# Kernel tuning notes

Measured on AMD Instinct MI355X. Metric: run time of the kernel, lower is better.

Reference implementation:

```python
import jax, jax.numpy as jnp
import numpy as np

B, C, CI, H, W = 4, 64, 32, 96, 96  # batch, in_channels, inter_channels, height, width


def conv2d(x, w, b, stride=1, pad=0):
    out = jax.lax.conv_general_dilated(
        x, w, (stride, stride), [(pad, pad), (pad, pad)],
        dimension_numbers=('NCHW', 'OIHW', 'NCHW'))
    return out + b[None, :, None, None]


def maxpool2(x):
    return jax.lax.reduce_window(x, -jnp.inf, jax.lax.max, (1, 1, 2, 2), (1, 1, 2, 2), 'VALID')


def up2(x):
    return jnp.repeat(jnp.repeat(x, 2, axis=2), 2, axis=3)


def bn_train(x, gamma, beta, eps=1e-5):
    # BatchNorm2d in training mode: batch statistics over (N, H, W)
    m = jnp.mean(x, axis=(0, 2, 3), keepdims=True)
    v = jnp.var(x, axis=(0, 2, 3), keepdims=True)
    return gamma[None, :, None, None] * (x - m) * jax.lax.rsqrt(v + eps) + beta[None, :, None, None]


def setup_inputs() -> dict:
    key = jax.random.key(0)
    ks = jax.random.split(key, 20)
    s1 = (2.0 / C) ** 0.5            # kaiming-ish for 1x1 convs
    s3 = (2.0 / (C * 9)) ** 0.5      # kaiming-ish for 3x3 convs
    sw = (2.0 / CI) ** 0.5
    return {
        'x':         jax.random.normal(ks[0], (B, C, H, W), jnp.float32),
        'x_pan':     jax.random.normal(ks[1], (B, C, H, W), jnp.float32),
        'g_w':       jax.random.normal(ks[2], (CI, C, 1, 1), jnp.float32) * s1,
        'g_b':       jnp.zeros((CI,), jnp.float32),
        'g_pan_w':   jax.random.normal(ks[3], (CI, C, 1, 1), jnp.float32) * s1,
        'g_pan_b':   jnp.zeros((CI,), jnp.float32),
        'theta_w':   jax.random.normal(ks[4], (CI, C, 3, 3), jnp.float32) * s3,
        'theta_b':   jax.random.normal(ks[5], (CI,), jnp.float32) * 0.02,
        'phi_w':     jax.random.normal(ks[6], (CI, C, 3, 3), jnp.float32) * s3,
        'phi_b':     jax.random.normal(ks[7], (CI,), jnp.float32) * 0.02,
        'phi_pan_w': jax.random.normal(ks[8], (CI, C, 3, 3), jnp.float32) * s3,
        'phi_pan_b': jax.random.normal(ks[9], (CI,), jnp.float32) * 0.02,
        'W_w':       jax.random.normal(ks[10], (C, CI, 1, 1), jnp.float32) * sw,
        'W_b':       jnp.zeros((C,), jnp.float32),
        'W_gamma':   jnp.ones((C,), jnp.float32),
        'W_beta':    jnp.zeros((C,), jnp.float32),
        'Wp_w':      jax.random.normal(ks[11], (C, CI, 1, 1), jnp.float32) * sw,
        'Wp_b':      jnp.zeros((C,), jnp.float32),
        'Wp_gamma':  jnp.ones((C,), jnp.float32),
        'Wp_beta':   jnp.zeros((C,), jnp.float32),
    }


def reference(x, x_pan, g_w, g_b, g_pan_w, g_pan_b, theta_w, theta_b,
              phi_w, phi_b, phi_pan_w, phi_pan_b,
              W_w, W_b, W_gamma, W_beta, Wp_w, Wp_b, Wp_gamma, Wp_beta):
    b = x.shape[0]
    # self branch
    g_x = maxpool2(conv2d(x, g_w, g_b)).reshape(b, CI, -1)                           # (B,CI,M)
    theta = up2(conv2d(x, theta_w, theta_b, stride=2, pad=1)).reshape(b, CI, -1)     # (B,CI,N)
    phi = up2(maxpool2(conv2d(x, phi_w, phi_b, stride=2, pad=1))).reshape(b, CI, -1) # (B,CI,M)
    f = jnp.einsum('bcn,bcm->bnm', theta, phi)                                       # (B,N,M)
    a = jax.nn.softmax(f, axis=-1)
    y = jnp.einsum('bnm,bcm->bcn', a, g_x).reshape(b, CI, H, W)
    W_y = bn_train(conv2d(y, W_w, W_b), W_gamma, W_beta)
    # cross-modal (pan) branch, sharing theta queries
    g_p = maxpool2(conv2d(x_pan, g_pan_w, g_pan_b)).reshape(b, CI, -1)
    phi_p = up2(maxpool2(conv2d(x_pan, phi_pan_w, phi_pan_b, stride=2, pad=1))).reshape(b, CI, -1)
    f_p = jnp.einsum('bcn,bcm->bnm', theta, phi_p)
    a_p = jax.nn.softmax(f_p, axis=-1)
    y_p = jnp.einsum('bnm,bcm->bcn', a_p, g_p).reshape(b, CI, H, W)
    Wp_y = bn_train(conv2d(y_p, Wp_w, Wp_b), Wp_gamma, Wp_beta)
    return jnp.concatenate([W_y, Wp_y], axis=1)  # (B, 2C, H, W)
```

## Files before the change

### kernel.cpp

```cpp
#include <hip/hip_runtime.h>
#include <math.h>

#define BB   4
#define CIN  64
#define CMID 32
#define HS   96
#define WS   96
#define H2   48
#define W2   48
#define H4   24
#define W4   24
#define N2   (H2*W2)
#define M4   (H4*W4)

__global__ __launch_bounds__(256) void conv3x3_kernel(
    const float* __restrict__ x, const float* __restrict__ x_pan,
    const float* __restrict__ theta_w, const float* __restrict__ theta_b,
    const float* __restrict__ phi_w,   const float* __restrict__ phi_b,
    const float* __restrict__ phi_pan_w, const float* __restrict__ phi_pan_b,
    float* __restrict__ T, float* __restrict__ Kp)
{
    const int p  = blockIdx.x;
    const int b  = blockIdx.y;
    const int cz = blockIdx.z;

    const float* xin  = (cz == 2) ? x_pan : x;
    const float* wgt  = (cz == 0) ? theta_w : (cz == 1 ? phi_w : phi_pan_w);
    const float* bias = (cz == 0) ? theta_b : (cz == 1 ? phi_b : phi_pan_b);

    __shared__ __align__(16) float xs[16][5][112];
    __shared__ float wsm[16][9][32];

    const int tid = threadIdx.x;
    const int co  = tid & 31;
    const int g   = tid >> 5;

    float acc[2][6];
    #pragma unroll
    for (int o = 0; o < 2; ++o)
        #pragma unroll
        for (int j = 0; j < 6; ++j) acc[o][j] = 0.f;

    const int row0 = 4*p - 1;

    for (int ci0 = 0; ci0 < CIN; ci0 += 16) {
        __syncthreads();
        for (int idx = tid; idx < 16*5*112; idx += 256) {
            int ci  = idx / (5*112);
            int rem = idx % (5*112);
            int rr  = rem / 112, cc = rem % 112;
            int row = row0 + rr, col = cc - 8;
            float v = 0.f;
            if (row >= 0 && row < HS && col >= 0 && col < WS)
                v = xin[((b*CIN + ci0 + ci)*HS + row)*WS + col];
            xs[ci][rr][cc] = v;
        }
        for (int idx = tid; idx < 16*9*32; idx += 256) {
            int c2 = idx & 31;
            int kk = (idx >> 5) % 9;
            int ci = idx / (9*32);
            wsm[ci][kk][c2] = wgt[(c2*CIN + ci0 + ci)*9 + kk];
        }
        __syncthreads();

        for (int ci = 0; ci < 16; ++ci) {
            float w9[9];
            #pragma unroll
            for (int kk = 0; kk < 9; ++kk) w9[kk] = wsm[ci][kk][co];

            #pragma unroll
            for (int rr = 0; rr < 5; ++rr) {
                const float4* xr = (const float4*)&xs[ci][rr][12*g + 4];
                float4 t0 = xr[0], t1 = xr[1], t2 = xr[2], t3 = xr[3];
                float xv[16] = {t0.x,t0.y,t0.z,t0.w, t1.x,t1.y,t1.z,t1.w,
                                t2.x,t2.y,t2.z,t2.w, t3.x,t3.y,t3.z,t3.w};
                if (rr <= 2) {
                    const int kh = rr;
                    #pragma unroll
                    for (int j = 0; j < 6; ++j)
                        #pragma unroll
                        for (int kw = 0; kw < 3; ++kw)
                            acc[0][j] += w9[kh*3+kw] * xv[3 + 2*j + kw];
                }
                if (rr >= 2) {
                    const int kh = rr - 2;
                    #pragma unroll
                    for (int j = 0; j < 6; ++j)
                        #pragma unroll
                        for (int kw = 0; kw < 3; ++kw)
                            acc[1][j] += w9[kh*3+kw] * xv[3 + 2*j + kw];
                }
            }
        }
    }

    const float bv = bias[co];
    if (cz == 0) {
        #pragma unroll
        for (int o = 0; o < 2; ++o)
            #pragma unroll
            for (int j = 0; j < 6; ++j)
                T[((b*CMID + co)*H2 + (2*p + o))*W2 + (6*g + j)] = acc[o][j] + bv;
    } else {
        #pragma unroll
        for (int j3 = 0; j3 < 3; ++j3) {
            float m = fmaxf(fmaxf(acc[0][2*j3], acc[0][2*j3+1]),
                            fmaxf(acc[1][2*j3], acc[1][2*j3+1]));
            Kp[((((cz-1)*BB + b)*CMID + co)*H4 + p)*W4 + (3*g + j3)] = m + bv;
        }
    }
}

__global__ __launch_bounds__(256) void gconv_kernel(
    const float* __restrict__ x, const float* __restrict__ x_pan,
    const float* __restrict__ g_w, const float* __restrict__ g_b,
    const float* __restrict__ g_pan_w, const float* __restrict__ g_pan_b,
    float* __restrict__ Vv)
{
    const int r4 = blockIdx.x;
    const int bb = blockIdx.y;
    const int br = bb >> 2, b = bb & 3;
    const float* xin = br ? x_pan : x;
    const float* wg  = br ? g_pan_w : g_w;
    const float* bg  = br ? g_pan_b : g_b;

    __shared__ float wl[CIN][CMID];
    const int tid = threadIdx.x;
    for (int idx = tid; idx < CIN*CMID; idx += 256) {
        int c = idx >> 6, ci = idx & 63;
        wl[ci][c] = wg[idx];
    }
    __syncthreads();

    const int c  = tid & 31;
    const int sg = tid >> 5;

    float acc[3][4][4];
    #pragma unroll
    for (int s = 0; s < 3; ++s)
        #pragma unroll
        for (int r = 0; r < 4; ++r)
            #pragma unroll
            for (int d = 0; d < 4; ++d) acc[s][r][d] = 0.f;

    for (int ci = 0; ci < CIN; ++ci) {
        const float wv = wl[ci][c];
        const float* xbase = &xin[((b*CIN + ci)*HS + 4*r4)*WS + 12*sg];
        #pragma unroll
        for (int r = 0; r < 4; ++r) {
            const float4* xp = (const float4*)(xbase + r*WS);
            #pragma unroll
            for (int s = 0; s < 3; ++s) {
                float4 xv = xp[s];
                acc[s][r][0] += wv*xv.x; acc[s][r][1] += wv*xv.y;
                acc[s][r][2] += wv*xv.z; acc[s][r][3] += wv*xv.w;
            }
        }
    }

    const float bv = bg[c];
    #pragma unroll
    for (int s = 0; s < 3; ++s) {
        float m00 = fmaxf(fmaxf(acc[s][0][0], acc[s][0][1]), fmaxf(acc[s][1][0], acc[s][1][1]));
        float m01 = fmaxf(fmaxf(acc[s][0][2], acc[s][0][3]), fmaxf(acc[s][1][2], acc[s][1][3]));
        float m10 = fmaxf(fmaxf(acc[s][2][0], acc[s][2][1]), fmaxf(acc[s][3][0], acc[s][3][1]));
        float m11 = fmaxf(fmaxf(acc[s][2][2], acc[s][2][3]), fmaxf(acc[s][3][2], acc[s][3][3]));
        Vv[((bb*CMID + c)*H4 + r4)*W4 + (3*sg + s)] = 0.25f*(m00+m01+m10+m11) + bv;
    }
}

__global__ __launch_bounds__(256) void attn_kernel(
    const float* __restrict__ T, const float* __restrict__ Kp,
    const float* __restrict__ Vv, float* __restrict__ Y)
{
    const int qt = blockIdx.x;
    const int bb = blockIdx.y;
    const int b  = bb & 3;

    __shared__ float smem[256*37];
    __shared__ float pmax[16][16];

    const int tid = threadIdx.x;
    const int ql  = tid & 15;
    const int ks  = tid >> 4;
    const int q   = qt*16 + ql;

    float qv[32];
    const float* Tb = T + b*CMID*N2;
    #pragma unroll
    for (int c = 0; c < 32; ++c) qv[c] = Tb[c*N2 + q];

    const float* Kb = Kp + bb*CMID*M4;
    const float* Vb = Vv + bb*CMID*M4;
    float* myss = &smem[tid*37];

    float m = -1e30f;
    for (int j = 0; j < 36; j += 4) {
        const int k = ks*36 + j;
        float s0 = 0.f, s1 = 0.f, s2 = 0.f, s3 = 0.f;
        #pragma unroll
        for (int c = 0; c < 32; ++c) {
            float4 kv = *(const float4*)&Kb[c*M4 + k];
            s0 += qv[c]*kv.x; s1 += qv[c]*kv.y; s2 += qv[c]*kv.z; s3 += qv[c]*kv.w;
        }
        myss[j] = s0; myss[j+1] = s1; myss[j+2] = s2; myss[j+3] = s3;
        m = fmaxf(m, fmaxf(fmaxf(s0, s1), fmaxf(s2, s3)));
    }
    pmax[ks][ql] = m;
    __syncthreads();
    float M = pmax[0][ql];
    #pragma unroll
    for (int i = 1; i < 16; ++i) M = fmaxf(M, pmax[i][ql]);

    float zp = 0.f;
    float av[32];
    #pragma unroll
    for (int c = 0; c < 32; ++c) av[c] = 0.f;
    for (int j = 0; j < 36; j += 4) {
        const int k = ks*36 + j;
        float p0 = __expf(myss[j]   - M);
        float p1 = __expf(myss[j+1] - M);
        float p2 = __expf(myss[j+2] - M);
        float p3 = __expf(myss[j+3] - M);
        zp += (p0 + p1) + (p2 + p3);
        #pragma unroll
        for (int c = 0; c < 32; ++c) {
            float4 vv = *(const float4*)&Vb[c*M4 + k];
            av[c] += p0*vv.x + p1*vv.y + p2*vv.z + p3*vv.w;
        }
    }
    __syncthreads();

    #pragma unroll
    for (int c = 0; c < 32; ++c) smem[tid*33 + c] = av[c];
    smem[256*33 + tid] = zp;
    __syncthreads();

    float Z = 0.f;
    #pragma unroll
    for (int i = 0; i < 16; ++i) Z += smem[256*33 + i*16 + ql];
    const float inv = 1.0f / Z;
    float* Yb = Y + bb*CMID*N2;
    #pragma unroll
    for (int cc = 0; cc < 2; ++cc) {
        const int c = ks*2 + cc;
        float sum = 0.f;
        #pragma unroll
        for (int i = 0; i < 16; ++i) sum += smem[(i*16 + ql)*33 + c];
        Yb[c*N2 + q] = sum * inv;
    }
}

__global__ __launch_bounds__(256) void wbn_kernel(
    const float* __restrict__ Y,
    const float* __restrict__ W_w, const float* __restrict__ W_b,
    const float* __restrict__ W_gamma, const float* __restrict__ W_beta,
    const float* __restrict__ Wp_w, const float* __restrict__ Wp_b,
    const float* __restrict__ Wp_gamma, const float* __restrict__ Wp_beta,
    float* __restrict__ out)
{
    const int og = blockIdx.x;
    const int br = og >> 6, o = og & 63;
    const float* Ww = br ? Wp_w : W_w;
    const float  bias = (br ? Wp_b : W_b)[o];
    const float* Ybase = Y + br*BB*CMID*N2;

    float wreg[32];
    #pragma unroll
    for (int c = 0; c < 32; ++c) wreg[c] = Ww[o*CMID + c];

    __shared__ float rbuf[256];
    const int tid = threadIdx.x;

    float4 zloc[9];
    float psum = 0.f;
    #pragma unroll
    for (int i = 0; i < 9; ++i) {
        const int g4 = tid + 256*i;
        const int b  = g4 / 576;
        const int n4 = (g4 % 576) * 4;
        const float* yb = Ybase + b*CMID*N2 + n4;
        float4 a = {0.f, 0.f, 0.f, 0.f};
        #pragma unroll
        for (int c = 0; c < 32; ++c) {
            float4 yv = *(const float4*)&yb[c*N2];
            a.x += wreg[c]*yv.x; a.y += wreg[c]*yv.y;
            a.z += wreg[c]*yv.z; a.w += wreg[c]*yv.w;
        }
        a.x += bias; a.y += bias; a.z += bias; a.w += bias;
        zloc[i] = a;
        psum += (a.x + a.y) + (a.z + a.w);
    }

    rbuf[tid] = psum;
    __syncthreads();
    for (int sft = 128; sft > 0; sft >>= 1) {
        if (tid < sft) rbuf[tid] += rbuf[tid + sft];
        __syncthreads();
    }
    const float mean = rbuf[0] * (1.0f/9216.0f);
    __syncthreads();

    float pvar = 0.f;
    #pragma unroll
    for (int i = 0; i < 9; ++i) {
        float4 a = zloc[i];
        float d0 = a.x - mean, d1 = a.y - mean, d2 = a.z - mean, d3 = a.w - mean;
        pvar += (d0*d0 + d1*d1) + (d2*d2 + d3*d3);
    }
    rbuf[tid] = pvar;
    __syncthreads();
    for (int sft = 128; sft > 0; sft >>= 1) {
        if (tid < sft) rbuf[tid] += rbuf[tid + sft];
        __syncthreads();
    }
    const float var = rbuf[0] * (1.0f/9216.0f);

    const float gamma = (br ? Wp_gamma : W_gamma)[o];
    const float beta  = (br ? Wp_beta  : W_beta)[o];
    const float scale = gamma * rsqrtf(var + 1e-5f);
    const float shift = beta - mean*scale;

    #pragma unroll
    for (int i = 0; i < 9; ++i) {
        const int g4 = tid + 256*i;
        const int b  = g4 / 576;
        const int nn = (g4 % 576) * 4;
        const int r  = nn / W2, s = nn % W2;
        float4 a = zloc[i];
        float v0 = a.x*scale + shift, v1 = a.y*scale + shift;
        float v2 = a.z*scale + shift, v3 = a.w*scale + shift;
        float4 lo = {v0, v0, v1, v1};
        float4 hi = {v2, v2, v3, v3};
        float* ob = out + ((size_t)(b*128 + og)*HS + 2*r)*WS + 2*s;
        *(float4*)(ob)        = lo;
        *(float4*)(ob + 4)    = hi;
        *(float4*)(ob + WS)   = lo;
        *(float4*)(ob + WS+4) = hi;
    }
}

extern "C" void kernel_launch(void* const* d_in, const int* in_sizes, int n_in,
                              void* d_out, int out_size, void* d_ws, size_t ws_size,
                              hipStream_t stream) {
    (void)in_sizes; (void)n_in; (void)out_size; (void)ws_size;
    const float* x         = (const float*)d_in[0];
    const float* x_pan     = (const float*)d_in[1];
    const float* g_w       = (const float*)d_in[2];
    const float* g_b       = (const float*)d_in[3];
    const float* g_pan_w   = (const float*)d_in[4];
    const float* g_pan_b   = (const float*)d_in[5];
    const float* theta_w   = (const float*)d_in[6];
    const float* theta_b   = (const float*)d_in[7];
    const float* phi_w     = (const float*)d_in[8];
    const float* phi_b     = (const float*)d_in[9];
    const float* phi_pan_w = (const float*)d_in[10];
    const float* phi_pan_b = (const float*)d_in[11];
    const float* W_w       = (const float*)d_in[12];
    const float* W_b       = (const float*)d_in[13];
    const float* W_gamma   = (const float*)d_in[14];
    const float* W_beta    = (const float*)d_in[15];
    const float* Wp_w      = (const float*)d_in[16];
    const float* Wp_b      = (const float*)d_in[17];
    const float* Wp_gamma  = (const float*)d_in[18];
    const float* Wp_beta   = (const float*)d_in[19];

    float* out = (float*)d_out;
    float* ws  = (float*)d_ws;

    float* T  = ws;
    float* Kp = T  + BB*CMID*N2;
    float* Vv = Kp + 2*BB*CMID*M4;
    float* Yw = Vv + 2*BB*CMID*M4;

    conv3x3_kernel<<<dim3(24, BB, 3), 256, 0, stream>>>(
        x, x_pan, theta_w, theta_b, phi_w, phi_b, phi_pan_w, phi_pan_b, T, Kp);
    gconv_kernel<<<dim3(24, 8), 256, 0, stream>>>(
        x, x_pan, g_w, g_b, g_pan_w, g_pan_b, Vv);
    attn_kernel<<<dim3(144, 8), 256, 0, stream>>>(T, Kp, Vv, Yw);
    wbn_kernel<<<dim3(128), 256, 0, stream>>>(
        Yw, W_w, W_b, W_gamma, W_beta, Wp_w, Wp_b, Wp_gamma, Wp_beta, out);
}
```

Measured before the change: 400.6 us.

## Restructure conv, attention and BN kernels for more parallelism and register reuse

The theta conv now computes only the needed stride-2 rows and writes T in a query-major layout. The phi convs are split by input-channel halves into partial buffers, which a new phipool kernel sums, max-pools and biases. The g conv stages inputs in shared memory over a larger grid. The attention kernel keeps scores in registers and reduces with wave shuffles instead of large shared arrays. The W conv plus BN is split into a parallel conv-with-partial-stats kernel and a normalize-and-upsample kernel using a sum/sum-of-squares variance. Together these are meant to raise occupancy and spread work over more blocks, at the cost of extra launches, intermediate traffic, and a less numerically stable variance formula.

```diff
diff --git a/kernel.cpp b/kernel.cpp
--- a/kernel.cpp
+++ b/kernel.cpp
@@ -16,17 +16,12 @@
 __global__ __launch_bounds__(256) void conv3x3_kernel(
     const float* __restrict__ x, const float* __restrict__ x_pan,
     const float* __restrict__ theta_w, const float* __restrict__ theta_b,
-    const float* __restrict__ phi_w,   const float* __restrict__ phi_b,
-    const float* __restrict__ phi_pan_w, const float* __restrict__ phi_pan_b,
-    float* __restrict__ T, float* __restrict__ Kp)
-{
-    const int p  = blockIdx.x;
+    const float* __restrict__ phi_w, const float* __restrict__ phi_pan_w,
+    float* __restrict__ T, float* __restrict__ Pphi)
+{
+    const int bx = blockIdx.x;
     const int b  = blockIdx.y;
     const int cz = blockIdx.z;
-
-    const float* xin  = (cz == 2) ? x_pan : x;
-    const float* wgt  = (cz == 0) ? theta_w : (cz == 1 ? phi_w : phi_pan_w);
-    const float* bias = (cz == 0) ? theta_b : (cz == 1 ? phi_b : phi_pan_b);
 
     __shared__ __align__(16) float xs[16][5][112];
     __shared__ float wsm[16][9][32];
@@ -35,141 +30,205 @@
     const int co  = tid & 31;
     const int g   = tid >> 5;
 
-    float acc[2][6];
-    #pragma unroll
-    for (int o = 0; o < 2; ++o)
-        #pragma unroll
-        for (int j = 0; j < 6; ++j) acc[o][j] = 0.f;
-
-    const int row0 = 4*p - 1;
-
-    for (int ci0 = 0; ci0 < CIN; ci0 += 16) {
-        __syncthreads();
-        for (int idx = tid; idx < 16*5*112; idx += 256) {
-            int ci  = idx / (5*112);
-            int rem = idx % (5*112);
-            int rr  = rem / 112, cc = rem % 112;
-            int row = row0 + rr, col = cc - 8;
-            float v = 0.f;
-            if (row >= 0 && row < HS && col >= 0 && col < WS)
-                v = xin[((b*CIN + ci0 + ci)*HS + row)*WS + col];
-            xs[ci][rr][cc] = v;
-        }
-        for (int idx = tid; idx < 16*9*32; idx += 256) {
-            int c2 = idx & 31;
-            int kk = (idx >> 5) % 9;
-            int ci = idx / (9*32);
-            wsm[ci][kk][c2] = wgt[(c2*CIN + ci0 + ci)*9 + kk];
-        }
-        __syncthreads();
-
-        for (int ci = 0; ci < 16; ++ci) {
-            float w9[9];
-            #pragma unroll
-            for (int kk = 0; kk < 9; ++kk) w9[kk] = wsm[ci][kk][co];
-
-            #pragma unroll
-            for (int rr = 0; rr < 5; ++rr) {
-                const float4* xr = (const float4*)&xs[ci][rr][12*g + 4];
-                float4 t0 = xr[0], t1 = xr[1], t2 = xr[2], t3 = xr[3];
-                float xv[16] = {t0.x,t0.y,t0.z,t0.w, t1.x,t1.y,t1.z,t1.w,
-                                t2.x,t2.y,t2.z,t2.w, t3.x,t3.y,t3.z,t3.w};
-                if (rr <= 2) {
-                    const int kh = rr;
+    const float* xin = (cz == 2) ? x_pan : x;
+    const float* wgt = (cz == 0) ? theta_w : (cz == 1 ? phi_w : phi_pan_w);
+
+    if (cz == 0) {
+        const int p = bx;
+        const int row0 = 2*p - 1;
+        float acc[6] = {0.f,0.f,0.f,0.f,0.f,0.f};
+
+        for (int ci0 = 0; ci0 < 64; ci0 += 16) {
+            __syncthreads();
+            for (int u = tid; u < 16*3*28; u += 256) {
+                int ci = u / 84, rem = u % 84, rr = rem / 28, k = rem % 28;
+                int row = row0 + rr;
+                float4 v = {0.f,0.f,0.f,0.f};
+                if (row >= 0 && k >= 2 && k <= 25)
+                    v = *(const float4*)&xin[((b*64 + ci0 + ci)*96 + row)*96 + 4*k - 8];
+                *(float4*)&xs[ci][rr][4*k] = v;
+            }
+            for (int u = tid; u < 1152; u += 256) {
+                int c2 = u / 36, f = u % 36;
+                float4 wv = *(const float4*)&wgt[c2*576 + ci0*9 + 4*f];
+                int lin = 4*f;
+                wsm[(lin  )/9][(lin  )%9][c2] = wv.x;
+                wsm[(lin+1)/9][(lin+1)%9][c2] = wv.y;
+                wsm[(lin+2)/9][(lin+2)%9][c2] = wv.z;
+                wsm[(lin+3)/9][(lin+3)%9][c2] = wv.w;
+            }
+            __syncthreads();
+
+            for (int ci = 0; ci < 16; ++ci) {
+                float w9[9];
+                #pragma unroll
+                for (int kk = 0; kk < 9; ++kk) w9[kk] = wsm[ci][kk][co];
+                #pragma unroll
+                for (int rr = 0; rr < 3; ++rr) {
+                    const float4* xr = (const float4*)&xs[ci][rr][12*g + 4];
+                    float4 t0 = xr[0], t1 = xr[1], t2 = xr[2], t3 = xr[3];
+                    float xv[16] = {t0.x,t0.y,t0.z,t0.w, t1.x,t1.y,t1.z,t1.w,
+                                    t2.x,t2.y,t2.z,t2.w, t3.x,t3.y,t3.z,t3.w};
                     #pragma unroll
                     for (int j = 0; j < 6; ++j)
                         #pragma unroll
                         for (int kw = 0; kw < 3; ++kw)
-                            acc[0][j] += w9[kh*3+kw] * xv[3 + 2*j + kw];
+                            acc[j] += w9[rr*3+kw] * xv[3 + 2*j + kw];
                 }
-                if (rr >= 2) {
-                    const int kh = rr - 2;
-                    #pragma unroll
-                    for (int j = 0; j < 6; ++j)
+            }
+        }
+        const float bv = theta_b[co];
+        #pragma unroll
+        for (int j = 0; j < 6; ++j)
+            T[(b*N2 + p*48 + 6*g + j)*32 + co] = acc[j] + bv;
+    } else {
+        const int p = bx >> 1, half = bx & 1;
+        const int row0 = 4*p - 1;
+        float acc[2][6];
+        #pragma unroll
+        for (int o = 0; o < 2; ++o)
+            #pragma unroll
+            for (int j = 0; j < 6; ++j) acc[o][j] = 0.f;
+
+        for (int cih = 0; cih < 2; ++cih) {
+            const int ci0 = half*32 + cih*16;
+            __syncthreads();
+            for (int u = tid; u < 16*5*28; u += 256) {
+                int ci = u / 140, rem = u % 140, rr = rem / 28, k = rem % 28;
+                int row = row0 + rr;
+                float4 v = {0.f,0.f,0.f,0.f};
+                if (row >= 0 && k >= 2 && k <= 25)
+                    v = *(const float4*)&xin[((b*64 + ci0 + ci)*96 + row)*96 + 4*k - 8];
+                *(float4*)&xs[ci][rr][4*k] = v;
+            }
+            for (int u = tid; u < 1152; u += 256) {
+                int c2 = u / 36, f = u % 36;
+                float4 wv = *(const float4*)&wgt[c2*576 + ci0*9 + 4*f];
+                int lin = 4*f;
+                wsm[(lin  )/9][(lin  )%9][c2] = wv.x;
+                wsm[(lin+1)/9][(lin+1)%9][c2] = wv.y;
+                wsm[(lin+2)/9][(lin+2)%9][c2] = wv.z;
+                wsm[(lin+3)/9][(lin+3)%9][c2] = wv.w;
+            }
+            __syncthreads();
+
+            for (int ci = 0; ci < 16; ++ci) {
+                float w9[9];
+                #pragma unroll
+                for (int kk = 0; kk < 9; ++kk) w9[kk] = wsm[ci][kk][co];
+                #pragma unroll
+                for (int rr = 0; rr < 5; ++rr) {
+                    const float4* xr = (const float4*)&xs[ci][rr][12*g + 4];
+                    float4 t0 = xr[0], t1 = xr[1], t2 = xr[2], t3 = xr[3];
+                    float xv[16] = {t0.x,t0.y,t0.z,t0.w, t1.x,t1.y,t1.z,t1.w,
+                                    t2.x,t2.y,t2.z,t2.w, t3.x,t3.y,t3.z,t3.w};
+                    if (rr <= 2) {
                         #pragma unroll
-                        for (int kw = 0; kw < 3; ++kw)
-                            acc[1][j] += w9[kh*3+kw] * xv[3 + 2*j + kw];
+                        for (int j = 0; j < 6; ++j)
+                            #pragma unroll
+                            for (int kw = 0; kw < 3; ++kw)
+                                acc[0][j] += w9[rr*3+kw] * xv[3 + 2*j + kw];
+                    }
+                    if (rr >= 2) {
+                        #pragma unroll
+                        for (int j = 0; j < 6; ++j)
+                            #pragma unroll
+                            for (int kw = 0; kw < 3; ++kw)
+                                acc[1][j] += w9[(rr-2)*3+kw] * xv[3 + 2*j + kw];
+                    }
                 }
             }
         }
-    }
-
-    const float bv = bias[co];
-    if (cz == 0) {
+        const int brn = cz - 1;
+        float* Pb = Pphi + (size_t)(((half*2 + brn)*4 + b)*32 + co)*N2;
         #pragma unroll
         for (int o = 0; o < 2; ++o)
             #pragma unroll
             for (int j = 0; j < 6; ++j)
-                T[((b*CMID + co)*H2 + (2*p + o))*W2 + (6*g + j)] = acc[o][j] + bv;
-    } else {
-        #pragma unroll
-        for (int j3 = 0; j3 < 3; ++j3) {
-            float m = fmaxf(fmaxf(acc[0][2*j3], acc[0][2*j3+1]),
-                            fmaxf(acc[1][2*j3], acc[1][2*j3+1]));
-            Kp[((((cz-1)*BB + b)*CMID + co)*H4 + p)*W4 + (3*g + j3)] = m + bv;
-        }
-    }
-}
-
-__global__ __launch_bounds__(256) void gconv_kernel(
+                Pb[(2*p + o)*48 + 6*g + j] = acc[o][j];
+    }
+}
+
+__global__ __launch_bounds__(256) void phipool_kernel(
+    const float* __restrict__ Pphi,
+    const float* __restrict__ phi_b, const float* __restrict__ phi_pan_b,
+    float* __restrict__ Kp)
+{
+    const int o = blockIdx.x*256 + threadIdx.x;
+    const int br   = o / 73728;
+    const int rem  = o % 73728;
+    const int b    = rem / 18432;
+    const int rem2 = rem % 18432;
+    const int co   = rem2 / 576;
+    const int rem3 = rem2 % 576;
+    const int pr   = rem3 / 24, pc = rem3 % 24;
+
+    const int h1 = 2*4*32*N2;
+    const int base = (((br*4 + b)*32 + co)*48 + 2*pr)*48 + 2*pc;
+    float2 a0 = *(const float2*)&Pphi[base];
+    float2 a1 = *(const float2*)&Pphi[base + 48];
+    float2 c0 = *(const float2*)&Pphi[h1 + base];
+    float2 c1 = *(const float2*)&Pphi[h1 + base + 48];
+    float v00 = a0.x + c0.x, v01 = a0.y + c0.y;
+    float v10 = a1.x + c1.x, v11 = a1.y + c1.y;
+    float bv = (br ? phi_pan_b : phi_b)[co];
+    Kp[o] = fmaxf(fmaxf(v00, v01), fmaxf(v10, v11)) + bv;
+}
+
+__global__ __launch_bounds__(384) void gconv_kernel(
     const float* __restrict__ x, const float* __restrict__ x_pan,
     const float* __restrict__ g_w, const float* __restrict__ g_b,
     const float* __restrict__ g_pan_w, const float* __restrict__ g_pan_b,
     float* __restrict__ Vv)
 {
     const int r4 = blockIdx.x;
-    const int bb = blockIdx.y;
+    const int ch = blockIdx.y;
+    const int bb = blockIdx.z;
     const int br = bb >> 2, b = bb & 3;
     const float* xin = br ? x_pan : x;
     const float* wg  = br ? g_pan_w : g_w;
-    const float* bg  = br ? g_pan_b : g_b;
-
-    __shared__ float wl[CIN][CMID];
+
+    __shared__ __align__(16) float xs[32][4][48];
+    __shared__ float wl[64*33];
     const int tid = threadIdx.x;
-    for (int idx = tid; idx < CIN*CMID; idx += 256) {
-        int c = idx >> 6, ci = idx & 63;
-        wl[ci][c] = wg[idx];
-    }
-    __syncthreads();
+    for (int u = tid; u < 2048; u += 384) {
+        int c2 = u >> 6, ci = u & 63;
+        wl[ci*33 + c2] = wg[u];
+    }
 
     const int c  = tid & 31;
-    const int sg = tid >> 5;
-
-    float acc[3][4][4];
-    #pragma unroll
-    for (int s = 0; s < 3; ++s)
-        #pragma unroll
-        for (int r = 0; r < 4; ++r)
-            #pragma unroll
-            for (int d = 0; d < 4; ++d) acc[s][r][d] = 0.f;
-
-    for (int ci = 0; ci < CIN; ++ci) {
-        const float wv = wl[ci][c];
-        const float* xbase = &xin[((b*CIN + ci)*HS + 4*r4)*WS + 12*sg];
-        #pragma unroll
-        for (int r = 0; r < 4; ++r) {
-            const float4* xp = (const float4*)(xbase + r*WS);
-            #pragma unroll
-            for (int s = 0; s < 3; ++s) {
-                float4 xv = xp[s];
-                acc[s][r][0] += wv*xv.x; acc[s][r][1] += wv*xv.y;
-                acc[s][r][2] += wv*xv.z; acc[s][r][3] += wv*xv.w;
-            }
-        }
-    }
-
-    const float bv = bg[c];
-    #pragma unroll
-    for (int s = 0; s < 3; ++s) {
-        float m00 = fmaxf(fmaxf(acc[s][0][0], acc[s][0][1]), fmaxf(acc[s][1][0], acc[s][1][1]));
-        float m01 = fmaxf(fmaxf(acc[s][0][2], acc[s][0][3]), fmaxf(acc[s][1][2], acc[s][1][3]));
-        float m10 = fmaxf(fmaxf(acc[s][2][0], acc[s][2][1]), fmaxf(acc[s][3][0], acc[s][3][1]));
-        float m11 = fmaxf(fmaxf(acc[s][2][2], acc[s][2][3]), fmaxf(acc[s][3][2], acc[s][3][3]));
-        Vv[((bb*CMID + c)*H4 + r4)*W4 + (3*sg + s)] = 0.25f*(m00+m01+m10+m11) + bv;
-    }
-}
-
-__global__ __launch_bounds__(256) void attn_kernel(
+    const int sl = tid >> 5;
+    float4 ac0 = {0,0,0,0}, ac1 = {0,0,0,0}, ac2 = {0,0,0,0}, ac3 = {0,0,0,0};
+
+    for (int ci0 = 0; ci0 < 64; ci0 += 32) {
+        __syncthreads();
+        for (int u = tid; u < 32*4*12; u += 384) {
+            int ci = u / 48, rem = u % 48, r = rem / 12, k = rem % 12;
+            *(float4*)&xs[ci][r][4*k] =
+                *(const float4*)&xin[((b*64 + ci0 + ci)*96 + 4*r4 + r)*96 + ch*48 + 4*k];
+        }
+        __syncthreads();
+        for (int ci = 0; ci < 32; ++ci) {
+            const float wv = wl[(ci0 + ci)*33 + c];
+            float4 x0 = *(const float4*)&xs[ci][0][4*sl];
+            float4 x1 = *(const float4*)&xs[ci][1][4*sl];
+            float4 x2 = *(const float4*)&xs[ci][2][4*sl];
+            float4 x3 = *(const float4*)&xs[ci][3][4*sl];
+            ac0.x += wv*x0.x; ac0.y += wv*x0.y; ac0.z += wv*x0.z; ac0.w += wv*x0.w;
+            ac1.x += wv*x1.x; ac1.y += wv*x1.y; ac1.z += wv*x1.z; ac1.w += wv*x1.w;
+            ac2.x += wv*x2.x; ac2.y += wv*x2.y; ac2.z += wv*x2.z; ac2.w += wv*x2.w;
+            ac3.x += wv*x3.x; ac3.y += wv*x3.y; ac3.z += wv*x3.z; ac3.w += wv*x3.w;
+        }
+    }
+    float m00 = fmaxf(fmaxf(ac0.x, ac0.y), fmaxf(ac1.x, ac1.y));
+    float m01 = fmaxf(fmaxf(ac0.z, ac0.w), fmaxf(ac1.z, ac1.w));
+    float m10 = fmaxf(fmaxf(ac2.x, ac2.y), fmaxf(ac3.x, ac3.y));
+    float m11 = fmaxf(fmaxf(ac2.z, ac2.w), fmaxf(ac3.z, ac3.w));
+    float bv = (br ? g_pan_b : g_b)[c];
+    Vv[(bb*32 + c)*576 + r4*24 + ch*12 + sl] = 0.25f*(m00+m01+m10+m11) + bv;
+}
+
+__global__ __launch_bounds__(256, 4) void attn_kernel(
     const float* __restrict__ T, const float* __restrict__ Kp,
     const float* __restrict__ Vv, float* __restrict__ Y)
 {
@@ -177,167 +236,170 @@
     const int bb = blockIdx.y;
     const int b  = bb & 3;
 
-    __shared__ float smem[256*37];
-    __shared__ float pmax[16][16];
-
-    const int tid = threadIdx.x;
-    const int ql  = tid & 15;
-    const int ks  = tid >> 4;
-    const int q   = qt*16 + ql;
+    __shared__ float mbuf[64];
+    __shared__ float zbuf[64];
+    __shared__ float avbuf[4*16*33];
+
+    const int tid  = threadIdx.x;
+    const int ql   = tid & 15;
+    const int ks   = tid >> 4;
+    const int q    = qt*16 + ql;
+    const int lane = tid & 63;
+    const int w    = tid >> 6;
 
     float qv[32];
-    const float* Tb = T + b*CMID*N2;
-    #pragma unroll
-    for (int c = 0; c < 32; ++c) qv[c] = Tb[c*N2 + q];
-
-    const float* Kb = Kp + bb*CMID*M4;
-    const float* Vb = Vv + bb*CMID*M4;
-    float* myss = &smem[tid*37];
-
+    const float4* Tq = (const float4*)(T + (size_t)(b*N2 + q)*32);
+    #pragma unroll
+    for (int i = 0; i < 8; ++i) {
+        float4 t = Tq[i];
+        qv[4*i] = t.x; qv[4*i+1] = t.y; qv[4*i+2] = t.z; qv[4*i+3] = t.w;
+    }
+
+    const float* Kb = Kp + (size_t)bb*32*576;
+    const float* Vb = Vv + (size_t)bb*32*576;
+
+    float sc[36];
     float m = -1e30f;
-    for (int j = 0; j < 36; j += 4) {
-        const int k = ks*36 + j;
+    #pragma unroll
+    for (int jj = 0; jj < 9; ++jj) {
+        const int k0 = ks*36 + 4*jj;
         float s0 = 0.f, s1 = 0.f, s2 = 0.f, s3 = 0.f;
         #pragma unroll
-        for (int c = 0; c < 32; ++c) {
-            float4 kv = *(const float4*)&Kb[c*M4 + k];
-            s0 += qv[c]*kv.x; s1 += qv[c]*kv.y; s2 += qv[c]*kv.z; s3 += qv[c]*kv.w;
-        }
-        myss[j] = s0; myss[j+1] = s1; myss[j+2] = s2; myss[j+3] = s3;
+        for (int c2 = 0; c2 < 32; ++c2) {
+            float4 kv = *(const float4*)&Kb[c2*576 + k0];
+            s0 += qv[c2]*kv.x; s1 += qv[c2]*kv.y; s2 += qv[c2]*kv.z; s3 += qv[c2]*kv.w;
+        }
+        sc[4*jj] = s0; sc[4*jj+1] = s1; sc[4*jj+2] = s2; sc[4*jj+3] = s3;
         m = fmaxf(m, fmaxf(fmaxf(s0, s1), fmaxf(s2, s3)));
     }
-    pmax[ks][ql] = m;
+    m = fmaxf(m, __shfl_xor(m, 16));
+    m = fmaxf(m, __shfl_xor(m, 32));
+    if (lane < 16) mbuf[w*16 + ql] = m;
     __syncthreads();
-    float M = pmax[0][ql];
-    #pragma unroll
-    for (int i = 1; i < 16; ++i) M = fmaxf(M, pmax[i][ql]);
-
+    const float M = fmaxf(fmaxf(mbuf[ql], mbuf[16+ql]),
+                          fmaxf(mbuf[32+ql], mbuf[48+ql]));
+
+    float av[32];
+    #pragma unroll
+    for (int c2 = 0; c2 < 32; ++c2) av[c2] = 0.f;
     float zp = 0.f;
-    float av[32];
-    #pragma unroll
-    for (int c = 0; c < 32; ++c) av[c] = 0.f;
-    for (int j = 0; j < 36; j += 4) {
-        const int k = ks*36 + j;
-        float p0 = __expf(myss[j]   - M);
-        float p1 = __expf(myss[j+1] - M);
-        float p2 = __expf(myss[j+2] - M);
-        float p3 = __expf(myss[j+3] - M);
+    #pragma unroll
+    for (int jj = 0; jj < 9; ++jj) {
+        const int k0 = ks*36 + 4*jj;
+        float p0 = __expf(sc[4*jj]   - M);
+        float p1 = __expf(sc[4*jj+1] - M);
+        float p2 = __expf(sc[4*jj+2] - M);
+        float p3 = __expf(sc[4*jj+3] - M);
         zp += (p0 + p1) + (p2 + p3);
         #pragma unroll
-        for (int c = 0; c < 32; ++c) {
-            float4 vv = *(const float4*)&Vb[c*M4 + k];
-            av[c] += p0*vv.x + p1*vv.y + p2*vv.z + p3*vv.w;
-        }
+        for (int c2 = 0; c2 < 32; ++c2) {
+            float4 vv = *(const float4*)&Vb[c2*576 + k0];
+            av[c2] += p0*vv.x + p1*vv.y + p2*vv.z + p3*vv.w;
+        }
+    }
+    zp += __shfl_xor(zp, 16); zp += __shfl_xor(zp, 32);
+    #pragma unroll
+    for (int c2 = 0; c2 < 32; ++c2) {
+        av[c2] += __shfl_xor(av[c2], 16);
+        av[c2] += __shfl_xor(av[c2], 32);
+    }
+    if (lane < 16) {
+        #pragma unroll
+        for (int c2 = 0; c2 < 32; ++c2) avbuf[(w*16 + ql)*33 + c2] = av[c2];
+        zbuf[w*16 + ql] = zp;
     }
     __syncthreads();
 
-    #pragma unroll
-    for (int c = 0; c < 32; ++c) smem[tid*33 + c] = av[c];
-    smem[256*33 + tid] = zp;
-    __syncthreads();
-
-    float Z = 0.f;
-    #pragma unroll
-    for (int i = 0; i < 16; ++i) Z += smem[256*33 + i*16 + ql];
+    const float Z = zbuf[ql] + zbuf[16+ql] + zbuf[32+ql] + zbuf[48+ql];
     const float inv = 1.0f / Z;
-    float* Yb = Y + bb*CMID*N2;
+    float* Yb = Y + (size_t)bb*32*N2;
     #pragma unroll
     for (int cc = 0; cc < 2; ++cc) {
-        const int c = ks*2 + cc;
-        float sum = 0.f;
-        #pragma unroll
-        for (int i = 0; i < 16; ++i) sum += smem[(i*16 + ql)*33 + c];
-        Yb[c*N2 + q] = sum * inv;
-    }
-}
-
-__global__ __launch_bounds__(256) void wbn_kernel(
+        const int c2 = 2*ks + cc;
+        float s = avbuf[ql*33 + c2] + avbuf[(16+ql)*33 + c2]
+                + avbuf[(32+ql)*33 + c2] + avbuf[(48+ql)*33 + c2];
+        Yb[c2*N2 + q] = s * inv;
+    }
+}
+
+__global__ __launch_bounds__(192) void wconv_kernel(
     const float* __restrict__ Y,
     const float* __restrict__ W_w, const float* __restrict__ W_b,
+    const float* __restrict__ Wp_w, const float* __restrict__ Wp_b,
+    float* __restrict__ zbuf, float* __restrict__ Psum, float* __restrict__ Psq)
+{
+    const int og = blockIdx.x, b = blockIdx.y;
+    const int br = og >> 6, o = og & 63;
+    const float* Ww = br ? Wp_w : W_w;
+    const float bias = (br ? Wp_b : W_b)[o];
+    const float* yb = Y + (size_t)(br*4 + b)*32*N2;
+
+    float wreg[32];
+    #pragma unroll
+    for (int c2 = 0; c2 < 32; ++c2) wreg[c2] = Ww[o*32 + c2];
+
+    const int tid = threadIdx.x;
+    float ps = 0.f, pq = 0.f;
+    float* zb = zbuf + (size_t)(og*4 + b)*N2;
+    #pragma unroll
+    for (int i = 0; i < 3; ++i) {
+        const int g = tid + 192*i;
+        float4 a = {bias, bias, bias, bias};
+        #pragma unroll
+        for (int c2 = 0; c2 < 32; ++c2) {
+            float4 yv = *(const float4*)&yb[c2*N2 + 4*g];
+            a.x += wreg[c2]*yv.x; a.y += wreg[c2]*yv.y;
+            a.z += wreg[c2]*yv.z; a.w += wreg[c2]*yv.w;
+        }
+        *(float4*)&zb[4*g] = a;
+        ps += (a.x + a.y) + (a.z + a.w);
+        pq += (a.x*a.x + a.y*a.y) + (a.z*a.z + a.w*a.w);
+    }
+    #pragma unroll
+    for (int d = 1; d < 64; d <<= 1) {
+        ps += __shfl_xor(ps, d);
+        pq += __shfl_xor(pq, d);
+    }
+    __shared__ float sb[3], qb[3];
+    const int lane = tid & 63, w = tid >> 6;
+    if (lane == 0) { sb[w] = ps; qb[w] = pq; }
+    __syncthreads();
+    if (tid == 0) {
+        Psum[og*4 + b] = sb[0] + sb[1] + sb[2];
+        Psq[og*4 + b]  = qb[0] + qb[1] + qb[2];
+    }
+}
+
+__global__ __launch_bounds__(576) void bnup_kernel(
+    const float* __restrict__ zbuf,
+    const float* __restrict__ Psum, const float* __restrict__ Psq,
     const float* __restrict__ W_gamma, const float* __restrict__ W_beta,
-    const float* __restrict__ Wp_w, const float* __restrict__ Wp_b,
     const float* __restrict__ Wp_gamma, const float* __restrict__ Wp_beta,
     float* __restrict__ out)
 {
-    const int og = blockIdx.x;
+    const int og = blockIdx.x, b = blockIdx.y;
     const int br = og >> 6, o = og & 63;
-    const float* Ww = br ? Wp_w : W_w;
-    const float  bias = (br ? Wp_b : W_b)[o];
-    const float* Ybase = Y + br*BB*CMID*N2;
-
-    float wreg[32];
-    #pragma unroll
-    for (int c = 0; c < 32; ++c) wreg[c] = Ww[o*CMID + c];
-
-    __shared__ float rbuf[256];
-    const int tid = threadIdx.x;
-
-    float4 zloc[9];
-    float psum = 0.f;
-    #pragma unroll
-    for (int i = 0; i < 9; ++i) {
-        const int g4 = tid + 256*i;
-        const int b  = g4 / 576;
-        const int n4 = (g4 % 576) * 4;
-        const float* yb = Ybase + b*CMID*N2 + n4;
-        float4 a = {0.f, 0.f, 0.f, 0.f};
-        #pragma unroll
-        for (int c = 0; c < 32; ++c) {
-            float4 yv = *(const float4*)&yb[c*N2];
-            a.x += wreg[c]*yv.x; a.y += wreg[c]*yv.y;
-            a.z += wreg[c]*yv.z; a.w += wreg[c]*yv.w;
-        }
-        a.x += bias; a.y += bias; a.z += bias; a.w += bias;
-        zloc[i] = a;
-        psum += (a.x + a.y) + (a.z + a.w);
-    }
-
-    rbuf[tid] = psum;
-    __syncthreads();
-    for (int sft = 128; sft > 0; sft >>= 1) {
-        if (tid < sft) rbuf[tid] += rbuf[tid + sft];
-        __syncthreads();
-    }
-    const float mean = rbuf[0] * (1.0f/9216.0f);
-    __syncthreads();
-
-    float pvar = 0.f;
-    #pragma unroll
-    for (int i = 0; i < 9; ++i) {
-        float4 a = zloc[i];
-        float d0 = a.x - mean, d1 = a.y - mean, d2 = a.z - mean, d3 = a.w - mean;
-        pvar += (d0*d0 + d1*d1) + (d2*d2 + d3*d3);
-    }
-    rbuf[tid] = pvar;
-    __syncthreads();
-    for (int sft = 128; sft > 0; sft >>= 1) {
-        if (tid < sft) rbuf[tid] += rbuf[tid + sft];
-        __syncthreads();
-    }
-    const float var = rbuf[0] * (1.0f/9216.0f);
-
+    const float s  = Psum[og*4] + Psum[og*4+1] + Psum[og*4+2] + Psum[og*4+3];
+    const float qq = Psq[og*4]  + Psq[og*4+1]  + Psq[og*4+2]  + Psq[og*4+3];
+    const float mean = s * (1.0f/9216.0f);
+    const float var  = qq * (1.0f/9216.0f) - mean*mean;
     const float gamma = (br ? Wp_gamma : W_gamma)[o];
     const float beta  = (br ? Wp_beta  : W_beta)[o];
     const float scale = gamma * rsqrtf(var + 1e-5f);
     const float shift = beta - mean*scale;
 
-    #pragma unroll
-    for (int i = 0; i < 9; ++i) {
-        const int g4 = tid + 256*i;
-        const int b  = g4 / 576;
-        const int nn = (g4 % 576) * 4;
-        const int r  = nn / W2, s = nn % W2;
-        float4 a = zloc[i];
-        float v0 = a.x*scale + shift, v1 = a.y*scale + shift;
-        float v2 = a.z*scale + shift, v3 = a.w*scale + shift;
-        float4 lo = {v0, v0, v1, v1};
-        float4 hi = {v2, v2, v3, v3};
-        float* ob = out + ((size_t)(b*128 + og)*HS + 2*r)*WS + 2*s;
-        *(float4*)(ob)        = lo;
-        *(float4*)(ob + 4)    = hi;
-        *(float4*)(ob + WS)   = lo;
-        *(float4*)(ob + WS+4) = hi;
-    }
+    const int t = threadIdx.x;
+    float4 a = *(const float4*)&zbuf[(size_t)(og*4 + b)*N2 + 4*t];
+    const int r = t / 12, cs = t % 12;
+    float v0 = a.x*scale + shift, v1 = a.y*scale + shift;
+    float v2 = a.z*scale + shift, v3 = a.w*scale + shift;
+    float4 lo = {v0, v0, v1, v1};
+    float4 hi = {v2, v2, v3, v3};
+    float* ob = out + ((size_t)(b*128 + og)*96 + 2*r)*96 + 8*cs;
+    *(float4*)(ob)      = lo;
+    *(float4*)(ob + 4)  = hi;
+    *(float4*)(ob + 96) = lo;
+    *(float4*)(ob + 100)= hi;
 }
 
 extern "C" void kernel_launch(void* const* d_in, const int* in_sizes, int n_in,
@@ -368,16 +430,23 @@
     float* out = (float*)d_out;
     float* ws  = (float*)d_ws;
 
-    float* T  = ws;
-    float* Kp = T  + BB*CMID*N2;
-    float* Vv = Kp + 2*BB*CMID*M4;
-    float* Yw = Vv + 2*BB*CMID*M4;
-
-    conv3x3_kernel<<<dim3(24, BB, 3), 256, 0, stream>>>(
-        x, x_pan, theta_w, theta_b, phi_w, phi_b, phi_pan_w, phi_pan_b, T, Kp);
-    gconv_kernel<<<dim3(24, 8), 256, 0, stream>>>(
+    float* T    = ws;
+    float* Kp   = T  + 294912;
+    float* Vv   = Kp + 147456;
+    float* Y    = Vv + 147456;
+    float* Pphi = Y  + 589824;
+    float* zbuf = Pphi;
+    float* Psum = Pphi + 1179648;
+    float* Psq  = Psum + 512;
+
+    conv3x3_kernel<<<dim3(48, 4, 3), 256, 0, stream>>>(
+        x, x_pan, theta_w, theta_b, phi_w, phi_pan_w, T, Pphi);
+    phipool_kernel<<<dim3(576), 256, 0, stream>>>(Pphi, phi_b, phi_pan_b, Kp);
+    gconv_kernel<<<dim3(24, 2, 8), 384, 0, stream>>>(
         x, x_pan, g_w, g_b, g_pan_w, g_pan_b, Vv);
-    attn_kernel<<<dim3(144, 8), 256, 0, stream>>>(T, Kp, Vv, Yw);
-    wbn_kernel<<<dim3(128), 256, 0, stream>>>(
-        Yw, W_w, W_b, W_gamma, W_beta, Wp_w, Wp_b, Wp_gamma, Wp_beta, out);
-}
+    attn_kernel<<<dim3(144, 8), 256, 0, stream>>>(T, Kp, Vv, Y);
+    wconv_kernel<<<dim3(128, 4), 192, 0, stream>>>(
+        Y, W_w, W_b, Wp_w, Wp_b, zbuf, Psum, Psq);
+    bnup_kernel<<<dim3(128, 4), 576, 0, stream>>>(
+        zbuf, Psum, Psq, W_gamma, W_beta, Wp_gamma, Wp_beta, out);
+}
```

After: 651.7 us. 1.63x slower.
